# Kernel tuning notes

Hardware: AMD Instinct MI355X
Metric: run time of the kernel (lower is better)

Reference implementation:

```python
import jax, jax.numpy as jnp
import numpy as np


def _get_pairs(top_k_centers):
    """Returns (p0, p1) int32 arrays of shape [B, S]: for each object a, the
    IoU-best partner a', ordered so the larger-L1 box comes first (as in source)."""
    cx, cy, h, w = jnp.split(top_k_centers, 4, axis=-1)  # [B,S,1] each, cxcyhw
    box = jnp.concatenate([cx - 0.5 * w, cy - 0.5 * h, cx + 0.5 * w, cy + 0.5 * h], axis=-1)  # [B,S,4] xyxy
    S = box.shape[1]
    b1 = box[:, :, None, :]  # [B,S,1,4]
    b2 = box[:, None, :, :]  # [B,1,S,4]
    inter_mins = jnp.maximum(b1[..., :2], b2[..., :2])
    inter_maxs = jnp.maximum(b1[..., 2:], b2[..., 2:])  # NOTE: source uses maximum here (kept faithful)
    inter_wh = jnp.clip(inter_maxs - inter_mins, 0.0)
    inter_area = inter_wh[..., 0] * inter_wh[..., 1]  # [B,S,S]
    area = (box[..., 2] - box[..., 0]) * (box[..., 3] - box[..., 1])  # [B,S]
    union = area[:, :, None] + area[:, None, :] - inter_area
    iou = inter_area / union - jnp.eye(S, dtype=inter_area.dtype)
    partner = jnp.argmax(iou, axis=-1)  # [B,S] int
    self_idx = jnp.broadcast_to(jnp.arange(S), partner.shape)
    l1 = jnp.abs(box[..., 2] - box[..., 0]) + jnp.abs(box[..., 3] - box[..., 1])  # [B,S]
    l1_partner = jnp.take_along_axis(l1, partner, axis=-1)
    keep = l1 >= l1_partner  # larger-L1 element goes first
    p0 = jnp.where(keep, self_idx, partner)
    p1 = jnp.where(keep, partner, self_idx)
    return p0, p1


def _gather_pair(a2, p):
    # a2: [B,H,S,S]; p: [B,S]. out[b,h,a,c] = a2[b,h,p[b,a],p[b,c]]
    rows = jnp.take_along_axis(a2, p[:, None, :, None], axis=2)
    return jnp.take_along_axis(rows, p[:, None, None, :], axis=3)


def setup_inputs() -> dict:
    key = jax.random.key(0)
    kq, kk, kv, kc = jax.random.split(key, 4)
    B, H, S, D = 8, 8, 1024, 64
    return {
        "query": jax.random.normal(kq, (B, H, S, D), dtype=jnp.float32),
        "key": jax.random.normal(kk, (B, H, S, D), dtype=jnp.float32),
        "value": jax.random.normal(kv, (B, H, S, D), dtype=jnp.float32),
        "top_k_centers": jax.random.uniform(kc, (B, S, 4), dtype=jnp.float32),
    }


def reference(query, key, value, top_k_centers):
    B, H, S, D = query.shape
    p0, p1 = _get_pairs(top_k_centers)
    # A2(a,b) = <q_{pi_a}, k_{pi_b}> + <q_{pi_a'}, k_{pi_b'}>
    a2 = jnp.einsum('bhqd,bhkd->bhqk', query, key)  # [B,H,S,S]
    scores = (_gather_pair(a2, p0) + _gather_pair(a2, p1)) * (1.0 / np.sqrt(2.0 * D))
    attn = jax.nn.softmax(scores, axis=-1)
    o2 = jnp.einsum('bhqk,bhkd->bhqd', attn, value)  # [B,H,S,D]
    return o2.transpose(0, 2, 1, 3).reshape(B, S, H * D)
```

## Files before the change

### kernel.cpp

```cpp
#include <hip/hip_runtime.h>
#include <hip/hip_bf16.h>

#define B_ 8
#define H_ 8
#define S_ 1024
#define D_ 64
#define QT 128
#define KT 64
#define NT (S_ / KT)

typedef float f32x16 __attribute__((ext_vector_type(16)));
typedef short s16x8 __attribute__((ext_vector_type(8)));
typedef unsigned int u32;

#define CSCALE ((float)(1.4426950408889634 / 11.313708498984761))

static __device__ __forceinline__ unsigned short f2bf(float f) {
    union { float f; unsigned u; } v; v.f = f;
    unsigned r = v.u + 0x7FFF + ((v.u >> 16) & 1);
    return (unsigned short)(r >> 16);
}

static __device__ __forceinline__ u32 cvtpk(float lo, float hi) {
    u32 r;
    asm("v_cvt_pk_bf16_f32 %0, %1, %2" : "=v"(r) : "v"(lo), "v"(hi));
    return r;
}

static __device__ __forceinline__ void glds16(const void* g, void* l) {
    __builtin_amdgcn_global_load_lds(
        (const __attribute__((address_space(1))) unsigned int*)(uintptr_t)g,
        (__attribute__((address_space(3))) unsigned int*)(unsigned)(uintptr_t)l,
        16, 0, 0);
}

__global__ __launch_bounds__(256) void pairs_kernel(const float* __restrict__ centers,
                                                    int* __restrict__ p0,
                                                    int* __restrict__ p1) {
#pragma clang fp contract(off)
    __shared__ float x0s[S_], y0s[S_], x1s[S_], y1s[S_], areas[S_], l1s[S_];
    const int b = blockIdx.y;
    const int t = threadIdx.x;
    for (int idx = t; idx < S_; idx += 256) {
        const float4 c = *reinterpret_cast<const float4*>(centers + ((size_t)b * S_ + idx) * 4);
        const float cx = c.x, cy = c.y, hh = c.z, ww = c.w;
        const float x0 = cx - 0.5f * ww;
        const float y0 = cy - 0.5f * hh;
        const float x1 = cx + 0.5f * ww;
        const float y1 = cy + 0.5f * hh;
        x0s[idx] = x0; y0s[idx] = y0; x1s[idx] = x1; y1s[idx] = y1;
        areas[idx] = (x1 - x0) * (y1 - y0);
        l1s[idx] = fabsf(x1 - x0) + fabsf(y1 - y0);
    }
    __syncthreads();
    const int i = blockIdx.x * 32 + (t >> 3);
    const int c8 = t & 7;
    const float x0i = x0s[i], y0i = y0s[i], x1i = x1s[i], y1i = y1s[i], ai = areas[i];
    float best = -1e38f; int arg = 0;
    const int j0 = c8 * 128;
    for (int j = j0; j < j0 + 128; ++j) {
        float wx = fmaxf(x1i, x1s[j]) - fmaxf(x0i, x0s[j]);
        float wy = fmaxf(y1i, y1s[j]) - fmaxf(y0i, y0s[j]);
        wx = fmaxf(wx, 0.0f);
        wy = fmaxf(wy, 0.0f);
        const float inter = wx * wy;
        const float uni = (ai + areas[j]) - inter;
        float v = inter / uni;
        if (j == i) v = v - 1.0f;
        if (v > best) { best = v; arg = j; }
    }
    #pragma unroll
    for (int m = 1; m <= 4; m <<= 1) {
        const float ob = __shfl_xor(best, m);
        const int oa = __shfl_xor(arg, m);
        if (ob > best || (ob == best && oa < arg)) { best = ob; arg = oa; }
    }
    if (c8 == 0) {
        const int partner = arg;
        const float l1i = l1s[i], l1p = l1s[partner];
        const int keep = (l1i >= l1p) ? 1 : 0;
        p0[b * S_ + i] = keep ? i : partner;
        p1[b * S_ + i] = keep ? partner : i;
    }
}

__global__ __launch_bounds__(256) void prep_kv(const float* __restrict__ k,
                                               const float* __restrict__ v,
                                               const int* __restrict__ p0,
                                               const int* __restrict__ p1,
                                               unsigned short* __restrict__ Kg,
                                               unsigned short* __restrict__ Vt) {
    __shared__ float tile[64][65];
    const int gid = blockIdx.x;
    const int stile = (gid >> 3) & 15;
    const int bh = ((gid >> 7) << 3) | (gid & 7);
    const int b = bh >> 3;
    const int s0 = stile * 64;
    const int t = threadIdx.x;
    {
        const float* kp = k + (size_t)bh * S_ * D_;
        const int* p0b = p0 + b * S_;
        const int* p1b = p1 + b * S_;
        const int chunk = t & 15;
        const int rsub = t >> 4;
        for (int it = 0; it < 4; ++it) {
            const int s = s0 + it * 16 + rsub;
            const int i0 = p0b[s], i1 = p1b[s];
            const float* src = (chunk < 8) ? (kp + (size_t)i0 * D_ + chunk * 8)
                                           : (kp + (size_t)i1 * D_ + (chunk - 8) * 8);
            const float4 f0 = *reinterpret_cast<const float4*>(src);
            const float4 f1 = *reinterpret_cast<const float4*>(src + 4);
            union { u32 u[4]; s16x8 v; } pk;
            pk.u[0] = cvtpk(f0.x, f0.y);
            pk.u[1] = cvtpk(f0.z, f0.w);
            pk.u[2] = cvtpk(f1.x, f1.y);
            pk.u[3] = cvtpk(f1.z, f1.w);
            unsigned short* row = Kg + ((size_t)bh * S_ + s) * 128;
            *reinterpret_cast<s16x8*>(row + (size_t)(chunk ^ (s & 7)) * 8) = pk.v;
        }
    }
    {
        const float* vp = v + ((size_t)bh * S_ + s0) * D_;
        const int row = t >> 2, cpart = (t & 3) * 16;
        for (int jj = 0; jj < 4; ++jj) {
            const float4 x = *reinterpret_cast<const float4*>(&vp[(size_t)row * D_ + cpart + jj * 4]);
            tile[row][cpart + jj * 4 + 0] = x.x;
            tile[row][cpart + jj * 4 + 1] = x.y;
            tile[row][cpart + jj * 4 + 2] = x.z;
            tile[row][cpart + jj * 4 + 3] = x.w;
        }
        __syncthreads();
        const int d = t >> 2;
        unsigned short* orow = Vt + ((size_t)bh * 64 + d) * S_ + s0;
        for (int cc = 0; cc < 2; ++cc) {
            const int chunk = (t & 3) * 2 + cc;
            unsigned short hh[8];
            for (int e = 0; e < 8; ++e) hh[e] = f2bf(tile[chunk * 8 + e][d]);
            const int chunk2 = chunk ^ (d & 7);
            *reinterpret_cast<s16x8*>(&orow[chunk2 * 8]) = *reinterpret_cast<s16x8*>(hh);
        }
    }
}

__global__ __launch_bounds__(256, 2) void attn_kernel(const float* __restrict__ q,
                                                      const unsigned short* __restrict__ Kg,
                                                      const unsigned short* __restrict__ Vt,
                                                      const int* __restrict__ p0,
                                                      const int* __restrict__ p1,
                                                      float* __restrict__ out) {
    __shared__ __align__(16) unsigned short Ks[3][KT][128];
    __shared__ __align__(16) unsigned short Vs[3][D_][KT];

    const int tid = threadIdx.x;
    const int w = tid >> 6;
    const int lane = tid & 63;
    const int qc = lane & 31;
    const int hi = lane >> 5;
    const int gid = blockIdx.x;
    const int qtile = (gid >> 3) & 7;
    const int bh = ((gid >> 6) << 3) | (gid & 7);
    const int b = bh >> 3;
    const int h = bh & 7;

    const float* qp = q + (size_t)bh * S_ * D_;
    const unsigned short* KgB = Kg + (size_t)bh * S_ * 128;
    const unsigned short* VtB = Vt + (size_t)bh * D_ * S_;

    s16x8 qf[8];
    {
        const int qr = qtile * QT + w * 32 + qc;
        const int i0 = p0[b * S_ + qr], i1 = p1[b * S_ + qr];
        #pragma unroll
        for (int p = 0; p < 8; ++p) {
            const int k0 = 16 * p + 8 * hi;
            const float* src = (p < 4) ? (qp + (size_t)i0 * D_ + k0)
                                       : (qp + (size_t)i1 * D_ + (k0 - 64));
            const float4 f0 = *reinterpret_cast<const float4*>(src);
            const float4 f1 = *reinterpret_cast<const float4*>(src + 4);
            union { u32 u[4]; s16x8 v; } pk;
            pk.u[0] = cvtpk(f0.x * CSCALE, f0.y * CSCALE);
            pk.u[1] = cvtpk(f0.z * CSCALE, f0.w * CSCALE);
            pk.u[2] = cvtpk(f1.x * CSCALE, f1.y * CSCALE);
            pk.u[3] = cvtpk(f1.z * CSCALE, f1.w * CSCALE);
            qf[p] = pk.v;
        }
    }

    const int rK = lane >> 4;
    const size_t cK = (size_t)(lane & 15) * 8;
    const int rV = lane >> 3;
    const size_t cV8 = (size_t)(lane & 7) * 8;
    auto STAGE = [&](int kt, int bf) {
        const size_t kbase = (size_t)(kt * KT) * 128;
        #pragma unroll
        for (int qq = 0; qq < 4; ++qq)
            glds16(KgB + kbase + ((size_t)((w * 4 + qq) * 4 + rK)) * 128 + cK,
                   &Ks[bf][(w * 4 + qq) * 4][0]);
        #pragma unroll
        for (int qq = 0; qq < 2; ++qq)
            glds16(VtB + ((size_t)((w * 2 + qq) * 8 + rV)) * S_ + (size_t)(kt * KT) + cV8,
                   &Vs[bf][(w * 2 + qq) * 8][0]);
    };
    STAGE(0, 0);
    STAGE(1, 1);

    f32x16 oacc0 = {}, oacc1 = {};
    float m_run = -1e30f, l_run = 0.0f;
    const int swz = qc & 7;
    int cur = 0, nxt2 = 2;

    for (int kt = 0; kt < NT; ++kt) {
        if (kt + 1 < NT) asm volatile("s_waitcnt vmcnt(6)" ::: "memory");
        else             asm volatile("s_waitcnt vmcnt(0)" ::: "memory");
        __builtin_amdgcn_s_barrier();
        if (kt + 2 < NT) STAGE(kt + 2, nxt2);

        const unsigned short(*KsC)[128] = Ks[cur];
        const unsigned short(*VsC)[KT] = Vs[cur];

        f32x16 st0 = {}, st1 = {};
        __builtin_amdgcn_s_setprio(1);
        #pragma unroll
        for (int p = 0; p < 8; ++p) {
            const int ch = (2 * p + hi) ^ swz;
            const s16x8 kf0 = *reinterpret_cast<const s16x8*>(&KsC[qc][ch * 8]);
            st0 = __builtin_amdgcn_mfma_f32_32x32x16_bf16(kf0, qf[p], st0, 0, 0, 0);
            const s16x8 kf1 = *reinterpret_cast<const s16x8*>(&KsC[32 + qc][ch * 8]);
            st1 = __builtin_amdgcn_mfma_f32_32x32x16_bf16(kf1, qf[p], st1, 0, 0, 0);
        }
        __builtin_amdgcn_s_setprio(0);

        float t16[16];
        #pragma unroll
        for (int i = 0; i < 16; ++i) t16[i] = fmaxf(st0[i], st1[i]);
        #pragma unroll
        for (int i = 0; i < 8; ++i) t16[i] = fmaxf(t16[i], t16[i + 8]);
        #pragma unroll
        for (int i = 0; i < 4; ++i) t16[i] = fmaxf(t16[i], t16[i + 4]);
        float mx = fmaxf(fmaxf(t16[0], t16[1]), fmaxf(t16[2], t16[3]));
        mx = fmaxf(mx, __shfl_xor(mx, 32));
        if (!__all(mx <= m_run + 8.0f)) {
            const float mn = fmaxf(m_run, mx);
            const float alpha = exp2f(m_run - mn);
            m_run = mn;
            l_run *= alpha;
            oacc0 *= alpha;
            oacc1 *= alpha;
        }
        #pragma unroll
        for (int i = 0; i < 16; ++i) {
            st0[i] = exp2f(st0[i] - m_run);
            st1[i] = exp2f(st1[i] - m_run);
        }
        float a16[16];
        #pragma unroll
        for (int i = 0; i < 16; ++i) a16[i] = st0[i] + st1[i];
        #pragma unroll
        for (int i = 0; i < 8; ++i) a16[i] += a16[i + 8];
        #pragma unroll
        for (int i = 0; i < 4; ++i) a16[i] += a16[i + 4];
        float ps = (a16[0] + a16[1]) + (a16[2] + a16[3]);
        ps += __shfl_xor(ps, 32);
        l_run += ps;

        u32 U0[8], U1[8];
        #pragma unroll
        for (int i = 0; i < 8; ++i) {
            U0[i] = cvtpk(st0[2 * i], st0[2 * i + 1]);
            U1[i] = cvtpk(st1[2 * i], st1[2 * i + 1]);
        }

        #pragma unroll
        for (int s = 0; s < 4; ++s) {
            const u32* Ut = (s < 2) ? U0 : U1;
            const int a = 4 * (s & 1);
            const u32 sendA = hi ? Ut[a] : Ut[a + 2];
            const u32 recvA = __shfl_xor(sendA, 32);
            const u32 w0 = hi ? recvA : Ut[a];
            const u32 w2 = hi ? Ut[a + 2] : recvA;
            const u32 sendB = hi ? Ut[a + 1] : Ut[a + 3];
            const u32 recvB = __shfl_xor(sendB, 32);
            const u32 w1 = hi ? recvB : Ut[a + 1];
            const u32 w3 = hi ? Ut[a + 3] : recvB;
            union { u32 u[4]; s16x8 v; } pf;
            pf.u[0] = w0; pf.u[1] = w1; pf.u[2] = w2; pf.u[3] = w3;
            const int ch = (2 * s + hi) ^ swz;
            __builtin_amdgcn_s_setprio(1);
            const s16x8 vf0 = *reinterpret_cast<const s16x8*>(&VsC[qc][ch * 8]);
            oacc0 = __builtin_amdgcn_mfma_f32_32x32x16_bf16(vf0, pf.v, oacc0, 0, 0, 0);
            const s16x8 vf1 = *reinterpret_cast<const s16x8*>(&VsC[32 + qc][ch * 8]);
            oacc1 = __builtin_amdgcn_mfma_f32_32x32x16_bf16(vf1, pf.v, oacc1, 0, 0, 0);
            __builtin_amdgcn_s_setprio(0);
        }
        cur = (cur + 1 == 3) ? 0 : cur + 1;
        nxt2 = (nxt2 + 1 == 3) ? 0 : nxt2 + 1;
    }

    const float invl = 1.0f / l_run;
    const int qrg = qtile * QT + w * 32 + qc;
    float* orow = out + ((size_t)b * S_ + qrg) * (H_ * D_) + h * D_;
    #pragma unroll
    for (int rq = 0; rq < 4; ++rq) {
        const float4 v0 = { oacc0[4 * rq] * invl, oacc0[4 * rq + 1] * invl,
                            oacc0[4 * rq + 2] * invl, oacc0[4 * rq + 3] * invl };
        *reinterpret_cast<float4*>(orow + 8 * rq + 4 * hi) = v0;
        const float4 v1 = { oacc1[4 * rq] * invl, oacc1[4 * rq + 1] * invl,
                            oacc1[4 * rq + 2] * invl, oacc1[4 * rq + 3] * invl };
        *reinterpret_cast<float4*>(orow + 32 + 8 * rq + 4 * hi) = v1;
    }
}

extern "C" void kernel_launch(void* const* d_in, const int* in_sizes, int n_in,
                              void* d_out, int out_size, void* d_ws, size_t ws_size,
                              hipStream_t stream) {
    (void)in_sizes; (void)n_in; (void)out_size; (void)ws_size;
    const float* q = (const float*)d_in[0];
    const float* k = (const float*)d_in[1];
    const float* v = (const float*)d_in[2];
    const float* c = (const float*)d_in[3];
    float* out = (float*)d_out;
    int* p0 = (int*)d_ws;
    int* p1 = p0 + B_ * S_;
    unsigned short* Kg = (unsigned short*)((char*)d_ws + 65536);
    unsigned short* Vt = Kg + (size_t)B_ * H_ * S_ * 128;
    pairs_kernel<<<dim3(32, 8), 256, 0, stream>>>(c, p0, p1);
    prep_kv<<<dim3(1024), 256, 0, stream>>>(k, v, p0, p1, Kg, Vt);
    attn_kernel<<<dim3(512), 256, 0, stream>>>(q, Kg, Vt, p0, p1, out);
}
```

Measured before the change: 81.66 us.

## Split K/V load waits, batch LDS fragment loads, double pairs-kernel parallelism

In the attention loop the single wait for the whole stage is replaced by finer vmcnt waits: one before the K reads, issued after the next stage's prefetch, and a later one before the V reads. This lets V loads keep landing while the QK MFMAs and softmax run. K and V fragments are now loaded into registers in batches before their MFMA chains. The online softmax is split into two per-subtile updates using vector max and sum helpers. The pairs kernel now uses 16 lanes per row and twice as many blocks. Risks are higher register pressure, which could cut occupancy, and vmcnt counts that must exactly match the number of loads issued per stage.

```diff
diff --git a/kernel.cpp b/kernel.cpp
--- a/kernel.cpp
+++ b/kernel.cpp
@@ -10,6 +10,8 @@
 #define NT (S_ / KT)
 
 typedef float f32x16 __attribute__((ext_vector_type(16)));
+typedef float f32x8v __attribute__((ext_vector_type(8)));
+typedef float f32x4v __attribute__((ext_vector_type(4)));
 typedef short s16x8 __attribute__((ext_vector_type(8)));
 typedef unsigned int u32;
 
@@ -25,6 +27,26 @@
     u32 r;
     asm("v_cvt_pk_bf16_f32 %0, %1, %2" : "=v"(r) : "v"(lo), "v"(hi));
     return r;
+}
+
+static __device__ __forceinline__ float vmax16(const f32x16 v) {
+    f32x8v a = __builtin_shufflevector(v, v, 0, 1, 2, 3, 4, 5, 6, 7);
+    f32x8v b = __builtin_shufflevector(v, v, 8, 9, 10, 11, 12, 13, 14, 15);
+    f32x8v m8 = __builtin_elementwise_max(a, b);
+    f32x4v c = __builtin_shufflevector(m8, m8, 0, 1, 2, 3);
+    f32x4v d = __builtin_shufflevector(m8, m8, 4, 5, 6, 7);
+    f32x4v m4 = __builtin_elementwise_max(c, d);
+    return fmaxf(fmaxf(m4[0], m4[1]), fmaxf(m4[2], m4[3]));
+}
+
+static __device__ __forceinline__ float vsum16(const f32x16 v) {
+    f32x8v a = __builtin_shufflevector(v, v, 0, 1, 2, 3, 4, 5, 6, 7);
+    f32x8v b = __builtin_shufflevector(v, v, 8, 9, 10, 11, 12, 13, 14, 15);
+    f32x8v s8 = a + b;
+    f32x4v c = __builtin_shufflevector(s8, s8, 0, 1, 2, 3);
+    f32x4v d = __builtin_shufflevector(s8, s8, 4, 5, 6, 7);
+    f32x4v s4 = c + d;
+    return (s4[0] + s4[1]) + (s4[2] + s4[3]);
 }
 
 static __device__ __forceinline__ void glds16(const void* g, void* l) {
@@ -53,12 +75,13 @@
         l1s[idx] = fabsf(x1 - x0) + fabsf(y1 - y0);
     }
     __syncthreads();
-    const int i = blockIdx.x * 32 + (t >> 3);
-    const int c8 = t & 7;
+    const int i = blockIdx.x * 16 + (t >> 4);
+    const int c16 = t & 15;
     const float x0i = x0s[i], y0i = y0s[i], x1i = x1s[i], y1i = y1s[i], ai = areas[i];
     float best = -1e38f; int arg = 0;
-    const int j0 = c8 * 128;
-    for (int j = j0; j < j0 + 128; ++j) {
+    const int j0 = c16 * 64;
+    #pragma unroll 4
+    for (int j = j0; j < j0 + 64; ++j) {
         float wx = fmaxf(x1i, x1s[j]) - fmaxf(x0i, x0s[j]);
         float wy = fmaxf(y1i, y1s[j]) - fmaxf(y0i, y0s[j]);
         wx = fmaxf(wx, 0.0f);
@@ -70,12 +93,12 @@
         if (v > best) { best = v; arg = j; }
     }
     #pragma unroll
-    for (int m = 1; m <= 4; m <<= 1) {
+    for (int m = 1; m <= 8; m <<= 1) {
         const float ob = __shfl_xor(best, m);
         const int oa = __shfl_xor(arg, m);
         if (ob > best || (ob == best && oa < arg)) { best = ob; arg = oa; }
     }
-    if (c8 == 0) {
+    if (c16 == 0) {
         const int partner = arg;
         const float l1i = l1s[i], l1p = l1s[partner];
         const int keep = (l1i >= l1p) ? 1 : 0;
@@ -210,58 +233,63 @@
     int cur = 0, nxt2 = 2;
 
     for (int kt = 0; kt < NT; ++kt) {
-        if (kt + 1 < NT) asm volatile("s_waitcnt vmcnt(6)" ::: "memory");
-        else             asm volatile("s_waitcnt vmcnt(0)" ::: "memory");
         __builtin_amdgcn_s_barrier();
         if (kt + 2 < NT) STAGE(kt + 2, nxt2);
 
+        if (kt + 2 < NT)      asm volatile("s_waitcnt vmcnt(14)" ::: "memory");
+        else if (kt + 1 < NT) asm volatile("s_waitcnt vmcnt(8)" ::: "memory");
+        else                  asm volatile("s_waitcnt vmcnt(2)" ::: "memory");
+
         const unsigned short(*KsC)[128] = Ks[cur];
         const unsigned short(*VsC)[KT] = Vs[cur];
 
+        s16x8 kf0[8], kf1[8];
+        #pragma unroll
+        for (int p = 0; p < 8; ++p) {
+            const int ch = (2 * p + hi) ^ swz;
+            kf0[p] = *reinterpret_cast<const s16x8*>(&KsC[qc][ch * 8]);
+            kf1[p] = *reinterpret_cast<const s16x8*>(&KsC[32 + qc][ch * 8]);
+        }
         f32x16 st0 = {}, st1 = {};
         __builtin_amdgcn_s_setprio(1);
         #pragma unroll
-        for (int p = 0; p < 8; ++p) {
-            const int ch = (2 * p + hi) ^ swz;
-            const s16x8 kf0 = *reinterpret_cast<const s16x8*>(&KsC[qc][ch * 8]);
-            st0 = __builtin_amdgcn_mfma_f32_32x32x16_bf16(kf0, qf[p], st0, 0, 0, 0);
-            const s16x8 kf1 = *reinterpret_cast<const s16x8*>(&KsC[32 + qc][ch * 8]);
-            st1 = __builtin_amdgcn_mfma_f32_32x32x16_bf16(kf1, qf[p], st1, 0, 0, 0);
-        }
+        for (int p = 0; p < 8; ++p)
+            st0 = __builtin_amdgcn_mfma_f32_32x32x16_bf16(kf0[p], qf[p], st0, 0, 0, 0);
+        #pragma unroll
+        for (int p = 0; p < 8; ++p)
+            st1 = __builtin_amdgcn_mfma_f32_32x32x16_bf16(kf1[p], qf[p], st1, 0, 0, 0);
         __builtin_amdgcn_s_setprio(0);
 
-        float t16[16];
-        #pragma unroll
-        for (int i = 0; i < 16; ++i) t16[i] = fmaxf(st0[i], st1[i]);
-        #pragma unroll
-        for (int i = 0; i < 8; ++i) t16[i] = fmaxf(t16[i], t16[i + 8]);
-        #pragma unroll
-        for (int i = 0; i < 4; ++i) t16[i] = fmaxf(t16[i], t16[i + 4]);
-        float mx = fmaxf(fmaxf(t16[0], t16[1]), fmaxf(t16[2], t16[3]));
-        mx = fmaxf(mx, __shfl_xor(mx, 32));
-        if (!__all(mx <= m_run + 8.0f)) {
-            const float mn = fmaxf(m_run, mx);
-            const float alpha = exp2f(m_run - mn);
-            m_run = mn;
-            l_run *= alpha;
-            oacc0 *= alpha;
-            oacc1 *= alpha;
-        }
-        #pragma unroll
-        for (int i = 0; i < 16; ++i) {
-            st0[i] = exp2f(st0[i] - m_run);
-            st1[i] = exp2f(st1[i] - m_run);
-        }
-        float a16[16];
-        #pragma unroll
-        for (int i = 0; i < 16; ++i) a16[i] = st0[i] + st1[i];
-        #pragma unroll
-        for (int i = 0; i < 8; ++i) a16[i] += a16[i + 8];
-        #pragma unroll
-        for (int i = 0; i < 4; ++i) a16[i] += a16[i + 4];
-        float ps = (a16[0] + a16[1]) + (a16[2] + a16[3]);
-        ps += __shfl_xor(ps, 32);
-        l_run += ps;
+        {
+            float mx = vmax16(st0);
+            mx = fmaxf(mx, __shfl_xor(mx, 32));
+            if (!__all(mx <= m_run + 8.0f)) {
+                const float mn = fmaxf(m_run, mx);
+                const float al = exp2f(m_run - mn);
+                m_run = mn; l_run *= al;
+                oacc0 *= al; oacc1 *= al;
+            }
+            #pragma unroll
+            for (int i = 0; i < 16; ++i) st0[i] = exp2f(st0[i] - m_run);
+            float ps = vsum16(st0);
+            ps += __shfl_xor(ps, 32);
+            l_run += ps;
+        }
+        {
+            float mx = vmax16(st1);
+            mx = fmaxf(mx, __shfl_xor(mx, 32));
+            if (!__all(mx <= m_run + 8.0f)) {
+                const float mn = fmaxf(m_run, mx);
+                const float al = exp2f(m_run - mn);
+                m_run = mn; l_run *= al;
+                oacc0 *= al; oacc1 *= al;
+            }
+            #pragma unroll
+            for (int i = 0; i < 16; ++i) st1[i] = exp2f(st1[i] - m_run);
+            float ps = vsum16(st1);
+            ps += __shfl_xor(ps, 32);
+            l_run += ps;
+        }
 
         u32 U0[8], U1[8];
         #pragma unroll
@@ -270,28 +298,43 @@
             U1[i] = cvtpk(st1[2 * i], st1[2 * i + 1]);
         }
 
+        u32 pfw[16];
         #pragma unroll
         for (int s = 0; s < 4; ++s) {
             const u32* Ut = (s < 2) ? U0 : U1;
             const int a = 4 * (s & 1);
             const u32 sendA = hi ? Ut[a] : Ut[a + 2];
+            const u32 sendB = hi ? Ut[a + 1] : Ut[a + 3];
             const u32 recvA = __shfl_xor(sendA, 32);
-            const u32 w0 = hi ? recvA : Ut[a];
-            const u32 w2 = hi ? Ut[a + 2] : recvA;
-            const u32 sendB = hi ? Ut[a + 1] : Ut[a + 3];
             const u32 recvB = __shfl_xor(sendB, 32);
-            const u32 w1 = hi ? recvB : Ut[a + 1];
-            const u32 w3 = hi ? Ut[a + 3] : recvB;
+            pfw[4 * s + 0] = hi ? recvA : Ut[a];
+            pfw[4 * s + 1] = hi ? recvB : Ut[a + 1];
+            pfw[4 * s + 2] = hi ? Ut[a + 2] : recvA;
+            pfw[4 * s + 3] = hi ? Ut[a + 3] : recvB;
+        }
+
+        if (kt + 2 < NT)      asm volatile("s_waitcnt vmcnt(12)" ::: "memory");
+        else if (kt + 1 < NT) asm volatile("s_waitcnt vmcnt(6)" ::: "memory");
+        else                  asm volatile("s_waitcnt vmcnt(0)" ::: "memory");
+
+        s16x8 vf0[4], vf1[4];
+        #pragma unroll
+        for (int s = 0; s < 4; ++s) {
+            const int ch = (2 * s + hi) ^ swz;
+            vf0[s] = *reinterpret_cast<const s16x8*>(&VsC[qc][ch * 8]);
+            vf1[s] = *reinterpret_cast<const s16x8*>(&VsC[32 + qc][ch * 8]);
+        }
+        __builtin_amdgcn_s_setprio(1);
+        #pragma unroll
+        for (int s = 0; s < 4; ++s) {
             union { u32 u[4]; s16x8 v; } pf;
-            pf.u[0] = w0; pf.u[1] = w1; pf.u[2] = w2; pf.u[3] = w3;
-            const int ch = (2 * s + hi) ^ swz;
-            __builtin_amdgcn_s_setprio(1);
-            const s16x8 vf0 = *reinterpret_cast<const s16x8*>(&VsC[qc][ch * 8]);
-            oacc0 = __builtin_amdgcn_mfma_f32_32x32x16_bf16(vf0, pf.v, oacc0, 0, 0, 0);
-            const s16x8 vf1 = *reinterpret_cast<const s16x8*>(&VsC[32 + qc][ch * 8]);
-            oacc1 = __builtin_amdgcn_mfma_f32_32x32x16_bf16(vf1, pf.v, oacc1, 0, 0, 0);
-            __builtin_amdgcn_s_setprio(0);
-        }
+            pf.u[0] = pfw[4 * s]; pf.u[1] = pfw[4 * s + 1];
+            pf.u[2] = pfw[4 * s + 2]; pf.u[3] = pfw[4 * s + 3];
+            oacc0 = __builtin_amdgcn_mfma_f32_32x32x16_bf16(vf0[s], pf.v, oacc0, 0, 0, 0);
+            oacc1 = __builtin_amdgcn_mfma_f32_32x32x16_bf16(vf1[s], pf.v, oacc1, 0, 0, 0);
+        }
+        __builtin_amdgcn_s_setprio(0);
+
         cur = (cur + 1 == 3) ? 0 : cur + 1;
         nxt2 = (nxt2 + 1 == 3) ? 0 : nxt2 + 1;
     }
@@ -323,7 +366,7 @@
     int* p1 = p0 + B_ * S_;
     unsigned short* Kg = (unsigned short*)((char*)d_ws + 65536);
     unsigned short* Vt = Kg + (size_t)B_ * H_ * S_ * 128;
-    pairs_kernel<<<dim3(32, 8), 256, 0, stream>>>(c, p0, p1);
+    pairs_kernel<<<dim3(64, 8), 256, 0, stream>>>(c, p0, p1);
     prep_kv<<<dim3(1024), 256, 0, stream>>>(k, v, p0, p1, Kg, Vt);
     attn_kernel<<<dim3(512), 256, 0, stream>>>(q, Kg, Vt, p0, p1, out);
 }
```

New measurement: 86.68 us. 1.06x slower.

## Split attention over KV halves with atomic-ticket merge and rework pairs kernel

Applied to the files above, without the earlier changes.

The attention kernel is split along the key dimension into two halves per query tile, doubling the grid from 512 to 1024 blocks. Each half writes its unnormalized output and (m, l) to a workspace slot, and the second block to finish merges the two using an atomic counter. The pipeline drops from triple to double buffering with plain __syncthreads, setprio hints are removed, and launch bounds are raised to 3 blocks per SM. The pairs kernel packs the box coordinates into float4 and uses 16 threads per row with a strided j loop. In exchange it adds a memset launch, partial-result traffic, and less latency hiding in the staging pipeline.

```diff
diff --git a/kernel.cpp b/kernel.cpp
--- a/kernel.cpp
+++ b/kernel.cpp
@@ -7,11 +7,22 @@
 #define D_ 64
 #define QT 128
 #define KT 64
-#define NT (S_ / KT)
 
 typedef float f32x16 __attribute__((ext_vector_type(16)));
 typedef short s16x8 __attribute__((ext_vector_type(8)));
 typedef unsigned int u32;
+
+#define OFF_P0   0
+#define OFF_P1   32768
+#define OFF_CNT  65536
+#define OFF_KG   131072
+#define KG_BYTES 16777216
+#define OFF_VT   (OFF_KG + KG_BYTES)
+#define VT_BYTES 8388608
+#define OFF_PART (OFF_VT + VT_BYTES)
+#define SLOT_F   8448
+#define PART_BYTES (1024ULL * SLOT_F * 4ULL)
+#define WS_NEED  ((size_t)OFF_PART + (size_t)PART_BYTES)
 
 #define CSCALE ((float)(1.4426950408889634 / 11.313708498984761))
 
@@ -38,7 +49,8 @@
                                                     int* __restrict__ p0,
                                                     int* __restrict__ p1) {
 #pragma clang fp contract(off)
-    __shared__ float x0s[S_], y0s[S_], x1s[S_], y1s[S_], areas[S_], l1s[S_];
+    __shared__ __align__(16) float4 box4[S_];
+    __shared__ float areas[S_], l1s[S_];
     const int b = blockIdx.y;
     const int t = threadIdx.x;
     for (int idx = t; idx < S_; idx += 256) {
@@ -48,34 +60,38 @@
         const float y0 = cy - 0.5f * hh;
         const float x1 = cx + 0.5f * ww;
         const float y1 = cy + 0.5f * hh;
-        x0s[idx] = x0; y0s[idx] = y0; x1s[idx] = x1; y1s[idx] = y1;
+        box4[idx] = float4{x0, y0, x1, y1};
         areas[idx] = (x1 - x0) * (y1 - y0);
         l1s[idx] = fabsf(x1 - x0) + fabsf(y1 - y0);
     }
     __syncthreads();
-    const int i = blockIdx.x * 32 + (t >> 3);
-    const int c8 = t & 7;
-    const float x0i = x0s[i], y0i = y0s[i], x1i = x1s[i], y1i = y1s[i], ai = areas[i];
+    const int i = blockIdx.x * 16 + (t >> 4);
+    const int c16 = t & 15;
+    const float4 bi = box4[i];
+    const float ai = areas[i];
     float best = -1e38f; int arg = 0;
-    const int j0 = c8 * 128;
-    for (int j = j0; j < j0 + 128; ++j) {
-        float wx = fmaxf(x1i, x1s[j]) - fmaxf(x0i, x0s[j]);
-        float wy = fmaxf(y1i, y1s[j]) - fmaxf(y0i, y0s[j]);
+    #pragma unroll 4
+    for (int it = 0; it < 64; ++it) {
+        const int j = it * 16 + c16;
+        const float4 bj = box4[j];
+        const float aj = areas[j];
+        float wx = fmaxf(bi.z, bj.z) - fmaxf(bi.x, bj.x);
+        float wy = fmaxf(bi.w, bj.w) - fmaxf(bi.y, bj.y);
         wx = fmaxf(wx, 0.0f);
         wy = fmaxf(wy, 0.0f);
         const float inter = wx * wy;
-        const float uni = (ai + areas[j]) - inter;
+        const float uni = (ai + aj) - inter;
         float v = inter / uni;
         if (j == i) v = v - 1.0f;
         if (v > best) { best = v; arg = j; }
     }
     #pragma unroll
-    for (int m = 1; m <= 4; m <<= 1) {
+    for (int m = 1; m <= 8; m <<= 1) {
         const float ob = __shfl_xor(best, m);
         const int oa = __shfl_xor(arg, m);
         if (ob > best || (ob == best && oa < arg)) { best = ob; arg = oa; }
     }
-    if (c8 == 0) {
+    if (c16 == 0) {
         const int partner = arg;
         const float l1i = l1s[i], l1p = l1s[partner];
         const int keep = (l1i >= l1p) ? 1 : 0;
@@ -142,14 +158,18 @@
     }
 }
 
-__global__ __launch_bounds__(256, 2) void attn_kernel(const float* __restrict__ q,
+template <bool SPLIT>
+__global__ __launch_bounds__(256, 3) void attn_kernel(const float* __restrict__ q,
                                                       const unsigned short* __restrict__ Kg,
                                                       const unsigned short* __restrict__ Vt,
                                                       const int* __restrict__ p0,
                                                       const int* __restrict__ p1,
+                                                      float* __restrict__ partial,
+                                                      int* __restrict__ cnt,
                                                       float* __restrict__ out) {
-    __shared__ __align__(16) unsigned short Ks[3][KT][128];
-    __shared__ __align__(16) unsigned short Vs[3][D_][KT];
+    __shared__ __align__(16) unsigned short Ks[2][KT][128];
+    __shared__ __align__(16) unsigned short Vs[2][D_][KT];
+    __shared__ int tick_sh;
 
     const int tid = threadIdx.x;
     const int w = tid >> 6;
@@ -158,13 +178,34 @@
     const int hi = lane >> 5;
     const int gid = blockIdx.x;
     const int qtile = (gid >> 3) & 7;
-    const int bh = ((gid >> 6) << 3) | (gid & 7);
+    const int half = SPLIT ? ((gid >> 6) & 1) : 0;
+    const int bh = SPLIT ? (((gid >> 7) << 3) | (gid & 7))
+                         : (((gid >> 6) << 3) | (gid & 7));
     const int b = bh >> 3;
     const int h = bh & 7;
+    const int kt0 = half * 8;
+    const int NTL = SPLIT ? 8 : 16;
 
     const float* qp = q + (size_t)bh * S_ * D_;
     const unsigned short* KgB = Kg + (size_t)bh * S_ * 128;
     const unsigned short* VtB = Vt + (size_t)bh * D_ * S_;
+
+    const int rK = lane >> 4;
+    const size_t cK = (size_t)(lane & 15) * 8;
+    const int rV = lane >> 3;
+    const size_t cV8 = (size_t)(lane & 7) * 8;
+    auto STAGE = [&](int gkt, int bf) {
+        const size_t kbase = (size_t)(gkt * KT) * 128;
+        #pragma unroll
+        for (int qq = 0; qq < 4; ++qq)
+            glds16(KgB + kbase + ((size_t)((w * 4 + qq) * 4 + rK)) * 128 + cK,
+                   &Ks[bf][(w * 4 + qq) * 4][0]);
+        #pragma unroll
+        for (int qq = 0; qq < 2; ++qq)
+            glds16(VtB + ((size_t)((w * 2 + qq) * 8 + rV)) * S_ + (size_t)(gkt * KT) + cV8,
+                   &Vs[bf][(w * 2 + qq) * 8][0]);
+    };
+    STAGE(kt0, 0);
 
     s16x8 qf[8];
     {
@@ -185,50 +226,25 @@
             qf[p] = pk.v;
         }
     }
-
-    const int rK = lane >> 4;
-    const size_t cK = (size_t)(lane & 15) * 8;
-    const int rV = lane >> 3;
-    const size_t cV8 = (size_t)(lane & 7) * 8;
-    auto STAGE = [&](int kt, int bf) {
-        const size_t kbase = (size_t)(kt * KT) * 128;
-        #pragma unroll
-        for (int qq = 0; qq < 4; ++qq)
-            glds16(KgB + kbase + ((size_t)((w * 4 + qq) * 4 + rK)) * 128 + cK,
-                   &Ks[bf][(w * 4 + qq) * 4][0]);
-        #pragma unroll
-        for (int qq = 0; qq < 2; ++qq)
-            glds16(VtB + ((size_t)((w * 2 + qq) * 8 + rV)) * S_ + (size_t)(kt * KT) + cV8,
-                   &Vs[bf][(w * 2 + qq) * 8][0]);
-    };
-    STAGE(0, 0);
-    STAGE(1, 1);
+    __syncthreads();
 
     f32x16 oacc0 = {}, oacc1 = {};
     float m_run = -1e30f, l_run = 0.0f;
     const int swz = qc & 7;
-    int cur = 0, nxt2 = 2;
-
-    for (int kt = 0; kt < NT; ++kt) {
-        if (kt + 1 < NT) asm volatile("s_waitcnt vmcnt(6)" ::: "memory");
-        else             asm volatile("s_waitcnt vmcnt(0)" ::: "memory");
-        __builtin_amdgcn_s_barrier();
-        if (kt + 2 < NT) STAGE(kt + 2, nxt2);
-
-        const unsigned short(*KsC)[128] = Ks[cur];
-        const unsigned short(*VsC)[KT] = Vs[cur];
+
+    for (int t = 0; t < NTL; ++t) {
+        const int bf = t & 1;
+        if (t + 1 < NTL) STAGE(kt0 + t + 1, bf ^ 1);
 
         f32x16 st0 = {}, st1 = {};
-        __builtin_amdgcn_s_setprio(1);
         #pragma unroll
         for (int p = 0; p < 8; ++p) {
             const int ch = (2 * p + hi) ^ swz;
-            const s16x8 kf0 = *reinterpret_cast<const s16x8*>(&KsC[qc][ch * 8]);
+            const s16x8 kf0 = *reinterpret_cast<const s16x8*>(&Ks[bf][qc][ch * 8]);
             st0 = __builtin_amdgcn_mfma_f32_32x32x16_bf16(kf0, qf[p], st0, 0, 0, 0);
-            const s16x8 kf1 = *reinterpret_cast<const s16x8*>(&KsC[32 + qc][ch * 8]);
+            const s16x8 kf1 = *reinterpret_cast<const s16x8*>(&Ks[bf][32 + qc][ch * 8]);
             st1 = __builtin_amdgcn_mfma_f32_32x32x16_bf16(kf1, qf[p], st1, 0, 0, 0);
         }
-        __builtin_amdgcn_s_setprio(0);
 
         float t16[16];
         #pragma unroll
@@ -241,11 +257,9 @@
         mx = fmaxf(mx, __shfl_xor(mx, 32));
         if (!__all(mx <= m_run + 8.0f)) {
             const float mn = fmaxf(m_run, mx);
-            const float alpha = exp2f(m_run - mn);
-            m_run = mn;
-            l_run *= alpha;
-            oacc0 *= alpha;
-            oacc1 *= alpha;
+            const float al = exp2f(m_run - mn);
+            m_run = mn; l_run *= al;
+            oacc0 *= al; oacc1 *= al;
         }
         #pragma unroll
         for (int i = 0; i < 16; ++i) {
@@ -285,45 +299,101 @@
             union { u32 u[4]; s16x8 v; } pf;
             pf.u[0] = w0; pf.u[1] = w1; pf.u[2] = w2; pf.u[3] = w3;
             const int ch = (2 * s + hi) ^ swz;
-            __builtin_amdgcn_s_setprio(1);
-            const s16x8 vf0 = *reinterpret_cast<const s16x8*>(&VsC[qc][ch * 8]);
+            const s16x8 vf0 = *reinterpret_cast<const s16x8*>(&Vs[bf][qc][ch * 8]);
             oacc0 = __builtin_amdgcn_mfma_f32_32x32x16_bf16(vf0, pf.v, oacc0, 0, 0, 0);
-            const s16x8 vf1 = *reinterpret_cast<const s16x8*>(&VsC[32 + qc][ch * 8]);
+            const s16x8 vf1 = *reinterpret_cast<const s16x8*>(&Vs[bf][32 + qc][ch * 8]);
             oacc1 = __builtin_amdgcn_mfma_f32_32x32x16_bf16(vf1, pf.v, oacc1, 0, 0, 0);
-            __builtin_amdgcn_s_setprio(0);
-        }
-        cur = (cur + 1 == 3) ? 0 : cur + 1;
-        nxt2 = (nxt2 + 1 == 3) ? 0 : nxt2 + 1;
-    }
-
-    const float invl = 1.0f / l_run;
-    const int qrg = qtile * QT + w * 32 + qc;
+        }
+        __syncthreads();
+    }
+
+    const int qrow = w * 32 + qc;
+    const int qrg = qtile * QT + qrow;
+
+    if (!SPLIT) {
+        const float invl = 1.0f / l_run;
+        float* orow = out + ((size_t)b * S_ + qrg) * (H_ * D_) + h * D_;
+        #pragma unroll
+        for (int rq = 0; rq < 4; ++rq) {
+            const float4 v0 = { oacc0[4 * rq] * invl, oacc0[4 * rq + 1] * invl,
+                                oacc0[4 * rq + 2] * invl, oacc0[4 * rq + 3] * invl };
+            *reinterpret_cast<float4*>(orow + 8 * rq + 4 * hi) = v0;
+            const float4 v1 = { oacc1[4 * rq] * invl, oacc1[4 * rq + 1] * invl,
+                                oacc1[4 * rq + 2] * invl, oacc1[4 * rq + 3] * invl };
+            *reinterpret_cast<float4*>(orow + 32 + 8 * rq + 4 * hi) = v1;
+        }
+        return;
+    }
+
+    const int pairIdx = bh * 8 + qtile;
+    const int mySlot = pairIdx * 2 + half;
+    float* slotO = partial + (size_t)mySlot * SLOT_F;
+    float* slotML = slotO + 8192;
+    #pragma unroll
+    for (int rq = 0; rq < 4; ++rq) {
+        *reinterpret_cast<float4*>(slotO + qrow * 64 + 8 * rq + 4 * hi) =
+            float4{ oacc0[4 * rq], oacc0[4 * rq + 1], oacc0[4 * rq + 2], oacc0[4 * rq + 3] };
+        *reinterpret_cast<float4*>(slotO + qrow * 64 + 32 + 8 * rq + 4 * hi) =
+            float4{ oacc1[4 * rq], oacc1[4 * rq + 1], oacc1[4 * rq + 2], oacc1[4 * rq + 3] };
+    }
+    if (hi == 0)
+        *reinterpret_cast<float2*>(slotML + qrow * 2) = float2{ m_run, l_run };
+    __threadfence();
+    __syncthreads();
+    if (tid == 0) tick_sh = atomicAdd(&cnt[pairIdx], 1);
+    __syncthreads();
+    if (tick_sh == 0) return;
+    __threadfence();
+
+    const float* pO = partial + (size_t)(pairIdx * 2 + (half ^ 1)) * SLOT_F;
+    const float* pML = pO + 8192;
+    const float2 ml = *reinterpret_cast<const float2*>(pML + qrow * 2);
+    const float M = fmaxf(m_run, ml.x);
+    const float wo = exp2f(m_run - M);
+    const float wp = exp2f(ml.x - M);
+    const float den = __fadd_rn(__fmul_rn(l_run, wo), __fmul_rn(ml.y, wp));
+    const float inv = 1.0f / den;
     float* orow = out + ((size_t)b * S_ + qrg) * (H_ * D_) + h * D_;
     #pragma unroll
     for (int rq = 0; rq < 4; ++rq) {
-        const float4 v0 = { oacc0[4 * rq] * invl, oacc0[4 * rq + 1] * invl,
-                            oacc0[4 * rq + 2] * invl, oacc0[4 * rq + 3] * invl };
-        *reinterpret_cast<float4*>(orow + 8 * rq + 4 * hi) = v0;
-        const float4 v1 = { oacc1[4 * rq] * invl, oacc1[4 * rq + 1] * invl,
-                            oacc1[4 * rq + 2] * invl, oacc1[4 * rq + 3] * invl };
-        *reinterpret_cast<float4*>(orow + 32 + 8 * rq + 4 * hi) = v1;
+        const float4 q0 = *reinterpret_cast<const float4*>(pO + qrow * 64 + 8 * rq + 4 * hi);
+        const float4 q1 = *reinterpret_cast<const float4*>(pO + qrow * 64 + 32 + 8 * rq + 4 * hi);
+        float4 o0, o1;
+        o0.x = __fadd_rn(__fmul_rn(oacc0[4 * rq + 0], wo), __fmul_rn(q0.x, wp)) * inv;
+        o0.y = __fadd_rn(__fmul_rn(oacc0[4 * rq + 1], wo), __fmul_rn(q0.y, wp)) * inv;
+        o0.z = __fadd_rn(__fmul_rn(oacc0[4 * rq + 2], wo), __fmul_rn(q0.z, wp)) * inv;
+        o0.w = __fadd_rn(__fmul_rn(oacc0[4 * rq + 3], wo), __fmul_rn(q0.w, wp)) * inv;
+        o1.x = __fadd_rn(__fmul_rn(oacc1[4 * rq + 0], wo), __fmul_rn(q1.x, wp)) * inv;
+        o1.y = __fadd_rn(__fmul_rn(oacc1[4 * rq + 1], wo), __fmul_rn(q1.y, wp)) * inv;
+        o1.z = __fadd_rn(__fmul_rn(oacc1[4 * rq + 2], wo), __fmul_rn(q1.z, wp)) * inv;
+        o1.w = __fadd_rn(__fmul_rn(oacc1[4 * rq + 3], wo), __fmul_rn(q1.w, wp)) * inv;
+        *reinterpret_cast<float4*>(orow + 8 * rq + 4 * hi) = o0;
+        *reinterpret_cast<float4*>(orow + 32 + 8 * rq + 4 * hi) = o1;
     }
 }
 
 extern "C" void kernel_launch(void* const* d_in, const int* in_sizes, int n_in,
                               void* d_out, int out_size, void* d_ws, size_t ws_size,
                               hipStream_t stream) {
-    (void)in_sizes; (void)n_in; (void)out_size; (void)ws_size;
+    (void)in_sizes; (void)n_in; (void)out_size;
     const float* q = (const float*)d_in[0];
     const float* k = (const float*)d_in[1];
     const float* v = (const float*)d_in[2];
     const float* c = (const float*)d_in[3];
     float* out = (float*)d_out;
-    int* p0 = (int*)d_ws;
-    int* p1 = p0 + B_ * S_;
-    unsigned short* Kg = (unsigned short*)((char*)d_ws + 65536);
-    unsigned short* Vt = Kg + (size_t)B_ * H_ * S_ * 128;
-    pairs_kernel<<<dim3(32, 8), 256, 0, stream>>>(c, p0, p1);
+    int* p0 = (int*)((char*)d_ws + OFF_P0);
+    int* p1 = (int*)((char*)d_ws + OFF_P1);
+    int* cnt = (int*)((char*)d_ws + OFF_CNT);
+    unsigned short* Kg = (unsigned short*)((char*)d_ws + OFF_KG);
+    unsigned short* Vt = (unsigned short*)((char*)d_ws + OFF_VT);
+    float* partial = (float*)((char*)d_ws + OFF_PART);
+
+    pairs_kernel<<<dim3(64, 8), 256, 0, stream>>>(c, p0, p1);
     prep_kv<<<dim3(1024), 256, 0, stream>>>(k, v, p0, p1, Kg, Vt);
-    attn_kernel<<<dim3(512), 256, 0, stream>>>(q, Kg, Vt, p0, p1, out);
-}
+    if (ws_size >= WS_NEED) {
+        hipMemsetAsync(cnt, 0, 512 * sizeof(int), stream);
+        attn_kernel<true><<<dim3(1024), 256, 0, stream>>>(q, Kg, Vt, p0, p1, partial, cnt, out);
+    } else {
+        attn_kernel<false><<<dim3(512), 256, 0, stream>>>(q, Kg, Vt, p0, p1, nullptr, nullptr, out);
+    }
+}
```

Measured after the change: 279.8 us. 3.43x slower.

## Pre-swizzle K/V into MFMA fragment order and load directly from global, dropping LDS staging

Applied to the files above, without the earlier changes.

prep_kv now writes gathered K and transposed V in a per-lane fragment layout, so each lane's MFMA operand sits in one contiguous 16-byte chunk. The attention kernel drops the LDS triple-buffer, the async global-to-LDS staging and the barriers, and reads K/V fragments straight from global memory (mostly from L2). Occupancy is raised to 3 blocks per CU. The pairs kernel uses packed float4 boxes in LDS, 16 lanes per row and twice as many blocks. The trade-off is that every wave now fetches its own copy of K/V from global instead of sharing it in LDS, and there is no explicit prefetch to hide that latency.

```diff
diff --git a/kernel.cpp b/kernel.cpp
--- a/kernel.cpp
+++ b/kernel.cpp
@@ -27,18 +27,12 @@
     return r;
 }
 
-static __device__ __forceinline__ void glds16(const void* g, void* l) {
-    __builtin_amdgcn_global_load_lds(
-        (const __attribute__((address_space(1))) unsigned int*)(uintptr_t)g,
-        (__attribute__((address_space(3))) unsigned int*)(unsigned)(uintptr_t)l,
-        16, 0, 0);
-}
-
 __global__ __launch_bounds__(256) void pairs_kernel(const float* __restrict__ centers,
                                                     int* __restrict__ p0,
                                                     int* __restrict__ p1) {
 #pragma clang fp contract(off)
-    __shared__ float x0s[S_], y0s[S_], x1s[S_], y1s[S_], areas[S_], l1s[S_];
+    __shared__ __align__(16) float4 box4[S_];
+    __shared__ float areas[S_], l1s[S_];
     const int b = blockIdx.y;
     const int t = threadIdx.x;
     for (int idx = t; idx < S_; idx += 256) {
@@ -48,34 +42,38 @@
         const float y0 = cy - 0.5f * hh;
         const float x1 = cx + 0.5f * ww;
         const float y1 = cy + 0.5f * hh;
-        x0s[idx] = x0; y0s[idx] = y0; x1s[idx] = x1; y1s[idx] = y1;
+        box4[idx] = float4{x0, y0, x1, y1};
         areas[idx] = (x1 - x0) * (y1 - y0);
         l1s[idx] = fabsf(x1 - x0) + fabsf(y1 - y0);
     }
     __syncthreads();
-    const int i = blockIdx.x * 32 + (t >> 3);
-    const int c8 = t & 7;
-    const float x0i = x0s[i], y0i = y0s[i], x1i = x1s[i], y1i = y1s[i], ai = areas[i];
+    const int i = blockIdx.x * 16 + (t >> 4);
+    const int c16 = t & 15;
+    const float4 bi = box4[i];
+    const float ai = areas[i];
     float best = -1e38f; int arg = 0;
-    const int j0 = c8 * 128;
-    for (int j = j0; j < j0 + 128; ++j) {
-        float wx = fmaxf(x1i, x1s[j]) - fmaxf(x0i, x0s[j]);
-        float wy = fmaxf(y1i, y1s[j]) - fmaxf(y0i, y0s[j]);
+    #pragma unroll 4
+    for (int it = 0; it < 64; ++it) {
+        const int j = it * 16 + c16;
+        const float4 bj = box4[j];
+        const float aj = areas[j];
+        float wx = fmaxf(bi.z, bj.z) - fmaxf(bi.x, bj.x);
+        float wy = fmaxf(bi.w, bj.w) - fmaxf(bi.y, bj.y);
         wx = fmaxf(wx, 0.0f);
         wy = fmaxf(wy, 0.0f);
         const float inter = wx * wy;
-        const float uni = (ai + areas[j]) - inter;
+        const float uni = (ai + aj) - inter;
         float v = inter / uni;
         if (j == i) v = v - 1.0f;
         if (v > best) { best = v; arg = j; }
     }
     #pragma unroll
-    for (int m = 1; m <= 4; m <<= 1) {
+    for (int m = 1; m <= 8; m <<= 1) {
         const float ob = __shfl_xor(best, m);
         const int oa = __shfl_xor(arg, m);
         if (ob > best || (ob == best && oa < arg)) { best = ob; arg = oa; }
     }
-    if (c8 == 0) {
+    if (c16 == 0) {
         const int partner = arg;
         const float l1i = l1s[i], l1p = l1s[partner];
         const int keep = (l1i >= l1p) ? 1 : 0;
@@ -101,13 +99,16 @@
         const float* kp = k + (size_t)bh * S_ * D_;
         const int* p0b = p0 + b * S_;
         const int* p1b = p1 + b * S_;
-        const int chunk = t & 15;
-        const int rsub = t >> 4;
+        unsigned short* Kt = Kg + (size_t)bh * (S_ * 128) + (size_t)stile * 8192;
         for (int it = 0; it < 4; ++it) {
-            const int s = s0 + it * 16 + rsub;
+            const int flat = it * 256 + t;
+            const int L = flat >> 6;
+            const int lane = flat & 63;
+            const int s = s0 + ((L >> 3) << 5) + (lane & 31);
+            const int c = ((L & 7) << 1) + (lane >> 5);
             const int i0 = p0b[s], i1 = p1b[s];
-            const float* src = (chunk < 8) ? (kp + (size_t)i0 * D_ + chunk * 8)
-                                           : (kp + (size_t)i1 * D_ + (chunk - 8) * 8);
+            const float* src = (c < 8) ? (kp + (size_t)i0 * D_ + c * 8)
+                                       : (kp + (size_t)i1 * D_ + (c - 8) * 8);
             const float4 f0 = *reinterpret_cast<const float4*>(src);
             const float4 f1 = *reinterpret_cast<const float4*>(src + 4);
             union { u32 u[4]; s16x8 v; } pk;
@@ -115,8 +116,7 @@
             pk.u[1] = cvtpk(f0.z, f0.w);
             pk.u[2] = cvtpk(f1.x, f1.y);
             pk.u[3] = cvtpk(f1.z, f1.w);
-            unsigned short* row = Kg + ((size_t)bh * S_ + s) * 128;
-            *reinterpret_cast<s16x8*>(row + (size_t)(chunk ^ (s & 7)) * 8) = pk.v;
+            *reinterpret_cast<s16x8*>(Kt + L * 512 + lane * 8) = pk.v;
         }
     }
     {
@@ -130,27 +130,27 @@
             tile[row][cpart + jj * 4 + 3] = x.w;
         }
         __syncthreads();
-        const int d = t >> 2;
-        unsigned short* orow = Vt + ((size_t)bh * 64 + d) * S_ + s0;
-        for (int cc = 0; cc < 2; ++cc) {
-            const int chunk = (t & 3) * 2 + cc;
+        unsigned short* Vtt = Vt + (size_t)bh * (S_ * D_) + (size_t)stile * 4096;
+        for (int it = 0; it < 2; ++it) {
+            const int flat = it * 256 + t;
+            const int L = flat >> 6;
+            const int lane = flat & 63;
+            const int kb = (((L & 3) << 1) + (lane >> 5)) * 8;
+            const int d = ((L >> 2) << 5) + (lane & 31);
             unsigned short hh[8];
-            for (int e = 0; e < 8; ++e) hh[e] = f2bf(tile[chunk * 8 + e][d]);
-            const int chunk2 = chunk ^ (d & 7);
-            *reinterpret_cast<s16x8*>(&orow[chunk2 * 8]) = *reinterpret_cast<s16x8*>(hh);
-        }
-    }
-}
-
-__global__ __launch_bounds__(256, 2) void attn_kernel(const float* __restrict__ q,
+            #pragma unroll
+            for (int e = 0; e < 8; ++e) hh[e] = f2bf(tile[kb + e][d]);
+            *reinterpret_cast<s16x8*>(Vtt + L * 512 + lane * 8) = *reinterpret_cast<s16x8*>(hh);
+        }
+    }
+}
+
+__global__ __launch_bounds__(256, 3) void attn_kernel(const float* __restrict__ q,
                                                       const unsigned short* __restrict__ Kg,
                                                       const unsigned short* __restrict__ Vt,
                                                       const int* __restrict__ p0,
                                                       const int* __restrict__ p1,
                                                       float* __restrict__ out) {
-    __shared__ __align__(16) unsigned short Ks[3][KT][128];
-    __shared__ __align__(16) unsigned short Vs[3][D_][KT];
-
     const int tid = threadIdx.x;
     const int w = tid >> 6;
     const int lane = tid & 63;
@@ -163,8 +163,8 @@
     const int h = bh & 7;
 
     const float* qp = q + (size_t)bh * S_ * D_;
-    const unsigned short* KgB = Kg + (size_t)bh * S_ * 128;
-    const unsigned short* VtB = Vt + (size_t)bh * D_ * S_;
+    const unsigned short* KgB = Kg + (size_t)bh * (S_ * 128) + (size_t)lane * 8;
+    const unsigned short* VtB = Vt + (size_t)bh * (S_ * D_) + (size_t)lane * 8;
 
     s16x8 qf[8];
     {
@@ -186,49 +186,29 @@
         }
     }
 
-    const int rK = lane >> 4;
-    const size_t cK = (size_t)(lane & 15) * 8;
-    const int rV = lane >> 3;
-    const size_t cV8 = (size_t)(lane & 7) * 8;
-    auto STAGE = [&](int kt, int bf) {
-        const size_t kbase = (size_t)(kt * KT) * 128;
-        #pragma unroll
-        for (int qq = 0; qq < 4; ++qq)
-            glds16(KgB + kbase + ((size_t)((w * 4 + qq) * 4 + rK)) * 128 + cK,
-                   &Ks[bf][(w * 4 + qq) * 4][0]);
-        #pragma unroll
-        for (int qq = 0; qq < 2; ++qq)
-            glds16(VtB + ((size_t)((w * 2 + qq) * 8 + rV)) * S_ + (size_t)(kt * KT) + cV8,
-                   &Vs[bf][(w * 2 + qq) * 8][0]);
-    };
-    STAGE(0, 0);
-    STAGE(1, 1);
-
     f32x16 oacc0 = {}, oacc1 = {};
     float m_run = -1e30f, l_run = 0.0f;
-    const int swz = qc & 7;
-    int cur = 0, nxt2 = 2;
 
     for (int kt = 0; kt < NT; ++kt) {
-        if (kt + 1 < NT) asm volatile("s_waitcnt vmcnt(6)" ::: "memory");
-        else             asm volatile("s_waitcnt vmcnt(0)" ::: "memory");
-        __builtin_amdgcn_s_barrier();
-        if (kt + 2 < NT) STAGE(kt + 2, nxt2);
-
-        const unsigned short(*KsC)[128] = Ks[cur];
-        const unsigned short(*VsC)[KT] = Vs[cur];
-
-        f32x16 st0 = {}, st1 = {};
-        __builtin_amdgcn_s_setprio(1);
-        #pragma unroll
-        for (int p = 0; p < 8; ++p) {
-            const int ch = (2 * p + hi) ^ swz;
-            const s16x8 kf0 = *reinterpret_cast<const s16x8*>(&KsC[qc][ch * 8]);
-            st0 = __builtin_amdgcn_mfma_f32_32x32x16_bf16(kf0, qf[p], st0, 0, 0, 0);
-            const s16x8 kf1 = *reinterpret_cast<const s16x8*>(&KsC[32 + qc][ch * 8]);
-            st1 = __builtin_amdgcn_mfma_f32_32x32x16_bf16(kf1, qf[p], st1, 0, 0, 0);
-        }
-        __builtin_amdgcn_s_setprio(0);
+        const unsigned short* Ktile = KgB + kt * 8192;
+        const unsigned short* Vtile = VtB + kt * 4096;
+
+        s16x8 kf[8];
+        #pragma unroll
+        for (int p = 0; p < 8; ++p)
+            kf[p] = *reinterpret_cast<const s16x8*>(Ktile + p * 512);
+        f32x16 st0 = {};
+        #pragma unroll
+        for (int p = 0; p < 8; ++p)
+            st0 = __builtin_amdgcn_mfma_f32_32x32x16_bf16(kf[p], qf[p], st0, 0, 0, 0);
+        __builtin_amdgcn_sched_barrier(0);
+        #pragma unroll
+        for (int p = 0; p < 8; ++p)
+            kf[p] = *reinterpret_cast<const s16x8*>(Ktile + (8 + p) * 512);
+        f32x16 st1 = {};
+        #pragma unroll
+        for (int p = 0; p < 8; ++p)
+            st1 = __builtin_amdgcn_mfma_f32_32x32x16_bf16(kf[p], qf[p], st1, 0, 0, 0);
 
         float t16[16];
         #pragma unroll
@@ -241,11 +221,9 @@
         mx = fmaxf(mx, __shfl_xor(mx, 32));
         if (!__all(mx <= m_run + 8.0f)) {
             const float mn = fmaxf(m_run, mx);
-            const float alpha = exp2f(m_run - mn);
-            m_run = mn;
-            l_run *= alpha;
-            oacc0 *= alpha;
-            oacc1 *= alpha;
+            const float al = exp2f(m_run - mn);
+            m_run = mn; l_run *= al;
+            oacc0 *= al; oacc1 *= al;
         }
         #pragma unroll
         for (int i = 0; i < 16; ++i) {
@@ -284,16 +262,11 @@
             const u32 w3 = hi ? Ut[a + 3] : recvB;
             union { u32 u[4]; s16x8 v; } pf;
             pf.u[0] = w0; pf.u[1] = w1; pf.u[2] = w2; pf.u[3] = w3;
-            const int ch = (2 * s + hi) ^ swz;
-            __builtin_amdgcn_s_setprio(1);
-            const s16x8 vf0 = *reinterpret_cast<const s16x8*>(&VsC[qc][ch * 8]);
+            const s16x8 vf0 = *reinterpret_cast<const s16x8*>(Vtile + s * 512);
             oacc0 = __builtin_amdgcn_mfma_f32_32x32x16_bf16(vf0, pf.v, oacc0, 0, 0, 0);
-            const s16x8 vf1 = *reinterpret_cast<const s16x8*>(&VsC[32 + qc][ch * 8]);
+            const s16x8 vf1 = *reinterpret_cast<const s16x8*>(Vtile + (4 + s) * 512);
             oacc1 = __builtin_amdgcn_mfma_f32_32x32x16_bf16(vf1, pf.v, oacc1, 0, 0, 0);
-            __builtin_amdgcn_s_setprio(0);
-        }
-        cur = (cur + 1 == 3) ? 0 : cur + 1;
-        nxt2 = (nxt2 + 1 == 3) ? 0 : nxt2 + 1;
+        }
     }
 
     const float invl = 1.0f / l_run;
@@ -323,7 +296,7 @@
     int* p1 = p0 + B_ * S_;
     unsigned short* Kg = (unsigned short*)((char*)d_ws + 65536);
     unsigned short* Vt = Kg + (size_t)B_ * H_ * S_ * 128;
-    pairs_kernel<<<dim3(32, 8), 256, 0, stream>>>(c, p0, p1);
+    pairs_kernel<<<dim3(64, 8), 256, 0, stream>>>(c, p0, p1);
     prep_kv<<<dim3(1024), 256, 0, stream>>>(k, v, p0, p1, Kg, Vt);
     attn_kernel<<<dim3(512), 256, 0, stream>>>(q, Kg, Vt, p0, p1, out);
 }
```

Measured after the change: 110.4 us. 35.2% more time.
